# Kernel tuning notes

Measured on AMD Instinct MI355X. Metric: run time of the kernel, lower is better.

Reference implementation:

```python
import jax, jax.numpy as jnp
import numpy as np

NUM_HEADS = 16


def setup_inputs() -> dict:
    key = jax.random.key(0)
    ks = jax.random.split(key, 8)
    B, S, D = 2, 2048, 1024
    scale = 1.0 / np.sqrt(D)
    return {
        "v": jax.random.normal(ks[0], (B, S, D), jnp.float32),
        "k": jax.random.normal(ks[1], (B, S, D), jnp.float32),
        "q": jax.random.normal(ks[2], (B, S, D), jnp.float32),
        "mask": jnp.zeros((B, S), dtype=bool),  # True = masked (padding)
        "Wq": jax.random.normal(ks[3], (D, D), jnp.float32) * scale,
        "bq": jnp.zeros((D,), jnp.float32),
        "Wk": jax.random.normal(ks[4], (D, D), jnp.float32) * scale,
        "bk": jnp.zeros((D,), jnp.float32),
        "Wv": jax.random.normal(ks[5], (D, D), jnp.float32) * scale,
        "bv": jnp.zeros((D,), jnp.float32),
    }


def reference(v, k, q, mask, Wq, bq, Wk, bk, Wv, bv):
    B, Sq, D = q.shape
    H = NUM_HEADS
    hd = D // H

    def proj(x, W, b):
        # torch Linear: x @ W.T + b ; then split heads -> [B, H, S, hd]
        y = jnp.einsum("bsd,ed->bse", x, W) + b
        return y.reshape(B, -1, H, hd).transpose(0, 2, 1, 3)

    qh = proj(q, Wq, bq)  # [B,H,Sq,hd]
    kh = proj(k, Wk, bk)  # [B,H,Sk,hd]
    vh = proj(v, Wv, bv)  # [B,H,Sk,hd]

    scores = jnp.einsum("bhqd,bhkd->bhqk", qh, kh) / jnp.sqrt(
        jnp.asarray(hd, jnp.float32)
    )
    m = mask[:, None, None, :]  # add_dims -> [B,1,1,Sk]
    scores = jnp.where(m, -jnp.inf, scores)
    w = jax.nn.softmax(scores, axis=-1)
    w = jnp.where(m, 0.0, w)

    out = jnp.einsum("bhqk,bhkd->bhqd", w, vh)
    return out.transpose(0, 2, 1, 3).reshape(B, Sq, D)
```

## Files before the change

kernel.cpp:

```cpp
#include <hip/hip_runtime.h>
#include <hip/hip_bf16.h>
#include <cstdint>

typedef __attribute__((ext_vector_type(8))) short bf16x8;
typedef __attribute__((ext_vector_type(4))) float f32x4;

#define PLDT 72
#define KLDT 72

static __device__ __forceinline__ unsigned short f2bf(float x) {
    __hip_bfloat16 h = __float2bfloat16(x);
    union { __hip_bfloat16 b; unsigned short u; } c; c.b = h; return c.u;
}
static __device__ __forceinline__ float bf2f(unsigned short b) {
    union { float f; uint32_t u; } v; v.u = ((uint32_t)b) << 16;
    return v.f;
}
static __device__ __forceinline__ float exp2b(float x) {
    return __builtin_amdgcn_exp2f(x);
}
static __device__ __forceinline__ unsigned int cvt_pk_bf16(float lo, float hi) {
    unsigned int r;
    asm("v_cvt_pk_bf16_f32 %0, %1, %2" : "=v"(r) : "v"(lo), "v"(hi));
    return r;
}
static __device__ __forceinline__ void gload_lds16(const unsigned short* g, unsigned short* l) {
    __builtin_amdgcn_global_load_lds(
        (const __attribute__((address_space(1))) void*)g,
        (__attribute__((address_space(3))) void*)l, 16, 0, 0);
}

__global__ __launch_bounds__(256) void cvt_all(
    const float* __restrict__ xq, const float* __restrict__ xk, const float* __restrict__ xv,
    const float* __restrict__ wq, const float* __restrict__ wk, const float* __restrict__ wv,
    unsigned short* __restrict__ oxq, unsigned short* __restrict__ oxk, unsigned short* __restrict__ oxv,
    unsigned short* __restrict__ owq, unsigned short* __restrict__ owk, unsigned short* __restrict__ owv) {
    const int z = blockIdx.z;
    const float* in = (z == 0) ? xq : (z == 1) ? xk : (z == 2) ? xv
                      : (z == 3) ? wq : (z == 4) ? wk : wv;
    unsigned short* out = (z == 0) ? oxq : (z == 1) ? oxk : (z == 2) ? oxv
                          : (z == 3) ? owq : (z == 4) ? owk : owv;
    const int n8 = (z < 3) ? 524288 : 131072;
    int i = blockIdx.x * 256 + threadIdx.x;
    if (i >= n8) return;
    const float4* ip = (const float4*)in;
    float4 a = ip[2 * i];
    float4 b = ip[2 * i + 1];
    uint4 r;
    r.x = cvt_pk_bf16(a.x, a.y);
    r.y = cvt_pk_bf16(a.z, a.w);
    r.z = cvt_pk_bf16(b.x, b.y);
    r.w = cvt_pk_bf16(b.z, b.w);
    *(uint4*)(out + (size_t)i * 8) = r;
}

__global__ __launch_bounds__(256) void proj_gemm_bf16(
    const unsigned short* __restrict__ Xqb, const unsigned short* __restrict__ Xkb,
    const unsigned short* __restrict__ Xvb,
    const unsigned short* __restrict__ Wqb, const unsigned short* __restrict__ Wkb,
    const unsigned short* __restrict__ Wvb,
    const float* __restrict__ bqp, const float* __restrict__ bkp, const float* __restrict__ bvp,
    unsigned short* __restrict__ dq, unsigned short* __restrict__ dk, unsigned short* __restrict__ dv) {
    __shared__ unsigned short a_lds[128 * 64];
    __shared__ unsigned short b_lds[128 * 64];

    const int z = blockIdx.z;
    const unsigned short* X = (z == 0) ? Xqb : (z == 1) ? Xkb : Xvb;
    const unsigned short* W = (z == 0) ? Wqb : (z == 1) ? Wkb : Wvb;
    const float* bias = (z == 0) ? bqp : (z == 1) ? bkp : bvp;
    unsigned short* dst = (z == 0) ? dq : (z == 1) ? dk : dv;
    const bool vtrans = (z == 2);

    const int tid = threadIdx.x;
    const int lane = tid & 63;
    const int w = tid >> 6;
    const int lr = lane & 15;
    const int lg = lane >> 4;
    const int m0 = blockIdx.x * 128;
    const int e0 = blockIdx.y * 128;
    const int wrow = (w >> 1) * 64;
    const int wcol = (w & 1) * 64;

    f32x4 acc[4][4] = {};

#pragma unroll 1
    for (int t = 0; t < 16; ++t) {
        const int k0 = t * 64;
        __syncthreads();
#pragma unroll
        for (int i = 0; i < 4; ++i) {
            int c = i * 256 + w * 64 + lane;
            int row = c >> 3;
            int col = (c & 7) * 8;
            gload_lds16(X + (size_t)(m0 + row) * 1024 + k0 + col,
                        a_lds + (size_t)(i * 256 + w * 64) * 8);
            gload_lds16(W + (size_t)(e0 + row) * 1024 + k0 + col,
                        b_lds + (size_t)(i * 256 + w * 64) * 8);
        }
        __syncthreads();

#pragma unroll
        for (int ks = 0; ks < 2; ++ks) {
            const int kk = ks * 32 + lg * 8;
            bf16x8 af[4], bfr[4];
#pragma unroll
            for (int mt = 0; mt < 4; ++mt)
                af[mt] = *(const bf16x8*)(a_lds + (wrow + mt * 16 + lr) * 64 + kk);
#pragma unroll
            for (int nt = 0; nt < 4; ++nt)
                bfr[nt] = *(const bf16x8*)(b_lds + (wcol + nt * 16 + lr) * 64 + kk);
            __builtin_amdgcn_s_setprio(1);
#pragma unroll
            for (int mt = 0; mt < 4; ++mt)
#pragma unroll
                for (int nt = 0; nt < 4; ++nt)
                    acc[mt][nt] = __builtin_amdgcn_mfma_f32_16x16x32_bf16(
                        af[mt], bfr[nt], acc[mt][nt], 0, 0, 0);
            __builtin_amdgcn_s_setprio(0);
        }
    }

    for (int mt = 0; mt < 4; ++mt)
        for (int nt = 0; nt < 4; ++nt)
            for (int i = 0; i < 4; ++i) {
                int m = m0 + wrow + mt * 16 + lg * 4 + i;
                int e = e0 + wcol + nt * 16 + lr;
                float val = acc[mt][nt][i] + bias[e];
                int b = m >> 11, s = m & 2047;
                int h = e >> 6, d = e & 63;
                if (vtrans)
                    dst[(((size_t)b * 16 + h) * 64 + d) * 2048 + s] = f2bf(val);
                else
                    dst[(((size_t)b * 16 + h) * 2048 + s) * 64 + d] = f2bf(val);
            }
}

__global__ __launch_bounds__(256) void attn_kernel(
    const unsigned short* __restrict__ Qh,
    const unsigned short* __restrict__ Kh,
    const unsigned short* __restrict__ VTh,
    const unsigned char* __restrict__ mask,
    float* __restrict__ Out) {
    __shared__ unsigned short k_lds[64 * KLDT];
    __shared__ unsigned short v_lds[64 * KLDT];
    __shared__ unsigned short pbuf[4][32 * PLDT];

    const int tid = threadIdx.x;
    const int lane = tid & 63;
    const int w = tid >> 6;
    const int lr = lane & 15;
    const int lg = lane >> 4;

    const int bid = blockIdx.x;
    const int wk = (bid & 7) * 64 + (bid >> 3);
    const int x = wk & 15;
    const int bh = wk >> 4;
    const int h = bh & 15;
    const int b = bh >> 4;
    const int q0 = x * 128;

    const size_t headoff = (((size_t)b * 16) + h) * 2048 * 64;
    const unsigned short* Qp = Qh + headoff;
    const unsigned short* Kp = Kh + headoff;
    const unsigned short* VTp = VTh + headoff;
    const unsigned char* maskp = mask + b * 2048;
    unsigned short* pw = pbuf[w];

    const int srow0 = tid >> 3;
    const int srow1 = srow0 + 32;
    const int sch = (tid & 7) * 8;

    const float qscale = 0.125f * 1.44269504088896340736f;
    bf16x8 qf[2][2];
#pragma unroll
    for (int qh = 0; qh < 2; ++qh) {
        int row = q0 + w * 32 + qh * 16 + lr;
#pragma unroll
        for (int ks = 0; ks < 2; ++ks) {
            bf16x8 t = *(const bf16x8*)(Qp + (size_t)row * 64 + ks * 32 + lg * 8);
#pragma unroll
            for (int j = 0; j < 8; ++j)
                t[j] = (short)f2bf(bf2f((unsigned short)t[j]) * qscale);
            qf[qh][ks] = t;
        }
    }

    f32x4 o[2][4] = {};
    float mrow[2] = {-INFINITY, -INFINITY};
    float lsum[2] = {0.f, 0.f};

    uint4 kr0 = *(const uint4*)(Kp + srow0 * 64 + sch);
    uint4 kr1 = *(const uint4*)(Kp + srow1 * 64 + sch);
    uint4 vr0 = *(const uint4*)(VTp + srow0 * 2048 + sch);
    uint4 vr1 = *(const uint4*)(VTp + srow1 * 2048 + sch);

#pragma unroll 1
    for (int t = 0; t < 32; ++t) {
        const int kv0 = t * 64;
        __syncthreads();
        *(uint4*)(k_lds + srow0 * KLDT + sch) = kr0;
        *(uint4*)(k_lds + srow1 * KLDT + sch) = kr1;
        *(uint4*)(v_lds + srow0 * KLDT + sch) = vr0;
        *(uint4*)(v_lds + srow1 * KLDT + sch) = vr1;
        __syncthreads();

        if (t < 31) {
            const int nv0 = kv0 + 64;
            kr0 = *(const uint4*)(Kp + (nv0 + srow0) * 64 + sch);
            kr1 = *(const uint4*)(Kp + (nv0 + srow1) * 64 + sch);
            vr0 = *(const uint4*)(VTp + srow0 * 2048 + nv0 + sch);
            vr1 = *(const uint4*)(VTp + srow1 * 2048 + nv0 + sch);
        }

        bf16x8 kf[2][4];
#pragma unroll
        for (int ks = 0; ks < 2; ++ks)
#pragma unroll
            for (int mt = 0; mt < 4; ++mt)
                kf[ks][mt] = *(const bf16x8*)(k_lds + (mt * 16 + lr) * KLDT + ks * 32 + lg * 8);

        f32x4 s[2][4] = {};
        __builtin_amdgcn_s_setprio(1);
#pragma unroll
        for (int ks = 0; ks < 2; ++ks)
#pragma unroll
            for (int mt = 0; mt < 4; ++mt) {
                s[0][mt] = __builtin_amdgcn_mfma_f32_16x16x32_bf16(kf[ks][mt], qf[0][ks], s[0][mt], 0, 0, 0);
                s[1][mt] = __builtin_amdgcn_mfma_f32_16x16x32_bf16(kf[ks][mt], qf[1][ks], s[1][mt], 0, 0, 0);
            }
        __builtin_amdgcn_s_setprio(0);

        unsigned long long mbits = __ballot(maskp[kv0 + lane] != 0);
        if (mbits) {
#pragma unroll
            for (int qh = 0; qh < 2; ++qh)
#pragma unroll
                for (int mt = 0; mt < 4; ++mt)
#pragma unroll
                    for (int i = 0; i < 4; ++i)
                        if ((mbits >> (mt * 16 + lg * 4 + i)) & 1ull) s[qh][mt][i] = -1e30f;
        }

#pragma unroll
        for (int qh = 0; qh < 2; ++qh) {
            float mx = s[qh][0][0];
#pragma unroll
            for (int mt = 0; mt < 4; ++mt)
#pragma unroll
                for (int i = 0; i < 4; ++i) mx = fmaxf(mx, s[qh][mt][i]);
            mx = fmaxf(mx, __shfl_xor(mx, 16));
            mx = fmaxf(mx, __shfl_xor(mx, 32));
            if (!__all(mx <= mrow[qh] + 8.0f)) {
                float nm = fmaxf(mrow[qh], mx);
                float f = exp2b(mrow[qh] - nm);
                mrow[qh] = nm;
                lsum[qh] *= f;
#pragma unroll
                for (int mt = 0; mt < 4; ++mt)
#pragma unroll
                    for (int i = 0; i < 4; ++i) o[qh][mt][i] *= f;
            }
            float p[4][4];
            float ls = 0.f;
#pragma unroll
            for (int mt = 0; mt < 4; ++mt)
#pragma unroll
                for (int i = 0; i < 4; ++i) {
                    p[mt][i] = exp2b(s[qh][mt][i] - mrow[qh]);
                    ls += p[mt][i];
                }
            ls += __shfl_xor(ls, 16);
            ls += __shfl_xor(ls, 32);
            lsum[qh] += ls;

#pragma unroll
            for (int mt = 0; mt < 4; ++mt) {
                uint2 pr;
                pr.x = cvt_pk_bf16(p[mt][0], p[mt][1]);
                pr.y = cvt_pk_bf16(p[mt][2], p[mt][3]);
                *(uint2*)(&pw[(qh * 16 + lr) * PLDT + mt * 16 + lg * 4]) = pr;
            }
        }

        bf16x8 vf[2][4];
#pragma unroll
        for (int ks = 0; ks < 2; ++ks)
#pragma unroll
            for (int mt = 0; mt < 4; ++mt)
                vf[ks][mt] = *(const bf16x8*)(v_lds + (mt * 16 + lr) * KLDT + ks * 32 + lg * 8);

        __builtin_amdgcn_s_setprio(1);
#pragma unroll
        for (int qh = 0; qh < 2; ++qh)
#pragma unroll
            for (int ks = 0; ks < 2; ++ks) {
                bf16x8 pfr = *(const bf16x8*)(&pw[(qh * 16 + lr) * PLDT + ks * 32 + lg * 8]);
#pragma unroll
                for (int mt = 0; mt < 4; ++mt)
                    o[qh][mt] = __builtin_amdgcn_mfma_f32_16x16x32_bf16(vf[ks][mt], pfr, o[qh][mt], 0, 0, 0);
            }
        __builtin_amdgcn_s_setprio(0);
    }

    float* ep = (float*)pw;
#pragma unroll
    for (int qh = 0; qh < 2; ++qh) {
        float rinv = 1.0f / lsum[qh];
#pragma unroll
        for (int mt = 0; mt < 4; ++mt)
#pragma unroll
            for (int i = 0; i < 4; ++i)
                ep[lr * 68 + mt * 16 + lg * 4 + i] = o[qh][mt][i] * rinv;
#pragma unroll
        for (int j = 0; j < 4; ++j) {
            int id = lane + 64 * j;
            int row = id >> 4;
            int c4 = (id & 15) << 2;
            float4 val = *(const float4*)(&ep[row * 68 + c4]);
            *(float4*)(&Out[((size_t)b * 2048 + q0 + w * 32 + qh * 16 + row) * 1024 + h * 64 + c4]) = val;
        }
    }
}

extern "C" void kernel_launch(void* const* d_in, const int* in_sizes, int n_in,
                              void* d_out, int out_size, void* d_ws, size_t ws_size,
                              hipStream_t stream) {
    const float* v = (const float*)d_in[0];
    const float* k = (const float*)d_in[1];
    const float* q = (const float*)d_in[2];
    const unsigned char* mask = (const unsigned char*)d_in[3];
    const float* Wq = (const float*)d_in[4];
    const float* bq = (const float*)d_in[5];
    const float* Wk = (const float*)d_in[6];
    const float* bk = (const float*)d_in[7];
    const float* Wv = (const float*)d_in[8];
    const float* bv = (const float*)d_in[9];
    float* out = (float*)d_out;

    unsigned short* ws = (unsigned short*)d_ws;
    unsigned short* qh  = ws;
    unsigned short* kh  = ws + 4194304;
    unsigned short* vT  = ws + 8388608;
    unsigned short* xqb = ws + 12582912;
    unsigned short* xkb = ws + 16777216;
    unsigned short* xvb = ws + 20971520;
    unsigned short* wqb = ws + 25165824;
    unsigned short* wkb = ws + 26214400;
    unsigned short* wvb = ws + 27262976;

    cvt_all<<<dim3(2048, 1, 6), 256, 0, stream>>>(q, k, v, Wq, Wk, Wv,
                                                  xqb, xkb, xvb, wqb, wkb, wvb);

    dim3 pgrid(32, 8, 3);
    proj_gemm_bf16<<<pgrid, 256, 0, stream>>>(xqb, xkb, xvb, wqb, wkb, wvb,
                                              bq, bk, bv, qh, kh, vT);

    attn_kernel<<<dim3(512), 256, 0, stream>>>(qh, kh, vT, mask, out);
}
```

Measured before the change: 125.2 us.

## Use 8 waves of 16 query rows each with double-buffered K/V LDS

The attention kernel now runs 512 threads per block. Each of 8 waves handles 16 query rows instead of 32, and every thread stages one K row chunk and one V row chunk. K/V LDS tiles are double-buffered, which removes one of the two __syncthreads per KV tile. The aim is more waves in flight to hide latency and less barrier cost. In exchange, each wave reuses K/V fragments across fewer query rows, so there is more LDS read traffic per unit of MFMA work.

```diff
diff --git a/kernel.cpp b/kernel.cpp
--- a/kernel.cpp
+++ b/kernel.cpp
@@ -135,15 +135,14 @@
             }
 }
 
-__global__ __launch_bounds__(256) void attn_kernel(
+__global__ __launch_bounds__(512) void attn_kernel(
     const unsigned short* __restrict__ Qh,
     const unsigned short* __restrict__ Kh,
     const unsigned short* __restrict__ VTh,
     const unsigned char* __restrict__ mask,
     float* __restrict__ Out) {
-    __shared__ unsigned short k_lds[64 * KLDT];
-    __shared__ unsigned short v_lds[64 * KLDT];
-    __shared__ unsigned short pbuf[4][32 * PLDT];
+    __shared__ unsigned short kv_lds[2][2][64 * KLDT];
+    __shared__ unsigned short pbuf[8][2176];
 
     const int tid = threadIdx.x;
     const int lane = tid & 63;
@@ -157,7 +156,7 @@
     const int bh = wk >> 4;
     const int h = bh & 15;
     const int b = bh >> 4;
-    const int q0 = x * 128;
+    const int q0 = x * 128 + w * 16;
 
     const size_t headoff = (((size_t)b * 16) + h) * 2048 * 64;
     const unsigned short* Qp = Qh + headoff;
@@ -166,120 +165,104 @@
     const unsigned char* maskp = mask + b * 2048;
     unsigned short* pw = pbuf[w];
 
-    const int srow0 = tid >> 3;
-    const int srow1 = srow0 + 32;
+    const int srow = tid >> 3;
     const int sch = (tid & 7) * 8;
 
     const float qscale = 0.125f * 1.44269504088896340736f;
-    bf16x8 qf[2][2];
-#pragma unroll
-    for (int qh = 0; qh < 2; ++qh) {
-        int row = q0 + w * 32 + qh * 16 + lr;
-#pragma unroll
-        for (int ks = 0; ks < 2; ++ks) {
-            bf16x8 t = *(const bf16x8*)(Qp + (size_t)row * 64 + ks * 32 + lg * 8);
-#pragma unroll
-            for (int j = 0; j < 8; ++j)
-                t[j] = (short)f2bf(bf2f((unsigned short)t[j]) * qscale);
-            qf[qh][ks] = t;
-        }
+    bf16x8 qf[2];
+#pragma unroll
+    for (int ks = 0; ks < 2; ++ks) {
+        bf16x8 t = *(const bf16x8*)(Qp + (size_t)(q0 + lr) * 64 + ks * 32 + lg * 8);
+#pragma unroll
+        for (int j = 0; j < 8; ++j)
+            t[j] = (short)f2bf(bf2f((unsigned short)t[j]) * qscale);
+        qf[ks] = t;
     }
 
-    f32x4 o[2][4] = {};
-    float mrow[2] = {-INFINITY, -INFINITY};
-    float lsum[2] = {0.f, 0.f};
-
-    uint4 kr0 = *(const uint4*)(Kp + srow0 * 64 + sch);
-    uint4 kr1 = *(const uint4*)(Kp + srow1 * 64 + sch);
-    uint4 vr0 = *(const uint4*)(VTp + srow0 * 2048 + sch);
-    uint4 vr1 = *(const uint4*)(VTp + srow1 * 2048 + sch);
+    f32x4 o[4] = {};
+    float mrow = -INFINITY;
+    float lsum = 0.f;
+
+    uint4 kr = *(const uint4*)(Kp + srow * 64 + sch);
+    uint4 vr = *(const uint4*)(VTp + srow * 2048 + sch);
+    int cur = 0;
 
 #pragma unroll 1
     for (int t = 0; t < 32; ++t) {
         const int kv0 = t * 64;
-        __syncthreads();
-        *(uint4*)(k_lds + srow0 * KLDT + sch) = kr0;
-        *(uint4*)(k_lds + srow1 * KLDT + sch) = kr1;
-        *(uint4*)(v_lds + srow0 * KLDT + sch) = vr0;
-        *(uint4*)(v_lds + srow1 * KLDT + sch) = vr1;
+        *(uint4*)(&kv_lds[cur][0][srow * KLDT + sch]) = kr;
+        *(uint4*)(&kv_lds[cur][1][srow * KLDT + sch]) = vr;
         __syncthreads();
 
         if (t < 31) {
             const int nv0 = kv0 + 64;
-            kr0 = *(const uint4*)(Kp + (nv0 + srow0) * 64 + sch);
-            kr1 = *(const uint4*)(Kp + (nv0 + srow1) * 64 + sch);
-            vr0 = *(const uint4*)(VTp + srow0 * 2048 + nv0 + sch);
-            vr1 = *(const uint4*)(VTp + srow1 * 2048 + nv0 + sch);
-        }
+            kr = *(const uint4*)(Kp + (nv0 + srow) * 64 + sch);
+            vr = *(const uint4*)(VTp + srow * 2048 + nv0 + sch);
+        }
+
+        const unsigned short* kb = &kv_lds[cur][0][0];
+        const unsigned short* vb = &kv_lds[cur][1][0];
 
         bf16x8 kf[2][4];
 #pragma unroll
         for (int ks = 0; ks < 2; ++ks)
 #pragma unroll
             for (int mt = 0; mt < 4; ++mt)
-                kf[ks][mt] = *(const bf16x8*)(k_lds + (mt * 16 + lr) * KLDT + ks * 32 + lg * 8);
-
-        f32x4 s[2][4] = {};
+                kf[ks][mt] = *(const bf16x8*)(kb + (mt * 16 + lr) * KLDT + ks * 32 + lg * 8);
+
+        f32x4 s[4] = {};
         __builtin_amdgcn_s_setprio(1);
 #pragma unroll
         for (int ks = 0; ks < 2; ++ks)
 #pragma unroll
-            for (int mt = 0; mt < 4; ++mt) {
-                s[0][mt] = __builtin_amdgcn_mfma_f32_16x16x32_bf16(kf[ks][mt], qf[0][ks], s[0][mt], 0, 0, 0);
-                s[1][mt] = __builtin_amdgcn_mfma_f32_16x16x32_bf16(kf[ks][mt], qf[1][ks], s[1][mt], 0, 0, 0);
-            }
+            for (int mt = 0; mt < 4; ++mt)
+                s[mt] = __builtin_amdgcn_mfma_f32_16x16x32_bf16(kf[ks][mt], qf[ks], s[mt], 0, 0, 0);
         __builtin_amdgcn_s_setprio(0);
 
         unsigned long long mbits = __ballot(maskp[kv0 + lane] != 0);
         if (mbits) {
 #pragma unroll
-            for (int qh = 0; qh < 2; ++qh)
-#pragma unroll
-                for (int mt = 0; mt < 4; ++mt)
-#pragma unroll
-                    for (int i = 0; i < 4; ++i)
-                        if ((mbits >> (mt * 16 + lg * 4 + i)) & 1ull) s[qh][mt][i] = -1e30f;
-        }
-
-#pragma unroll
-        for (int qh = 0; qh < 2; ++qh) {
-            float mx = s[qh][0][0];
-#pragma unroll
-            for (int mt = 0; mt < 4; ++mt)
-#pragma unroll
-                for (int i = 0; i < 4; ++i) mx = fmaxf(mx, s[qh][mt][i]);
-            mx = fmaxf(mx, __shfl_xor(mx, 16));
-            mx = fmaxf(mx, __shfl_xor(mx, 32));
-            if (!__all(mx <= mrow[qh] + 8.0f)) {
-                float nm = fmaxf(mrow[qh], mx);
-                float f = exp2b(mrow[qh] - nm);
-                mrow[qh] = nm;
-                lsum[qh] *= f;
-#pragma unroll
-                for (int mt = 0; mt < 4; ++mt)
-#pragma unroll
-                    for (int i = 0; i < 4; ++i) o[qh][mt][i] *= f;
+            for (int mt = 0; mt < 4; ++mt)
+#pragma unroll
+                for (int i = 0; i < 4; ++i)
+                    if ((mbits >> (mt * 16 + lg * 4 + i)) & 1ull) s[mt][i] = -1e30f;
+        }
+
+        float mx = fmaxf(fmaxf(fmaxf(s[0][0], s[0][1]), fmaxf(s[0][2], s[0][3])),
+                         fmaxf(fmaxf(s[1][0], s[1][1]), fmaxf(s[1][2], s[1][3])));
+        mx = fmaxf(mx, fmaxf(fmaxf(fmaxf(s[2][0], s[2][1]), fmaxf(s[2][2], s[2][3])),
+                             fmaxf(fmaxf(s[3][0], s[3][1]), fmaxf(s[3][2], s[3][3]))));
+        mx = fmaxf(mx, __shfl_xor(mx, 16));
+        mx = fmaxf(mx, __shfl_xor(mx, 32));
+        if (!__all(mx <= mrow + 8.0f)) {
+            float nm = fmaxf(mrow, mx);
+            float f = exp2b(mrow - nm);
+            mrow = nm;
+            lsum *= f;
+#pragma unroll
+            for (int mt = 0; mt < 4; ++mt)
+#pragma unroll
+                for (int i = 0; i < 4; ++i) o[mt][i] *= f;
+        }
+        float p[4][4];
+        float ls = 0.f;
+#pragma unroll
+        for (int mt = 0; mt < 4; ++mt)
+#pragma unroll
+            for (int i = 0; i < 4; ++i) {
+                p[mt][i] = exp2b(s[mt][i] - mrow);
+                ls += p[mt][i];
             }
-            float p[4][4];
-            float ls = 0.f;
-#pragma unroll
-            for (int mt = 0; mt < 4; ++mt)
-#pragma unroll
-                for (int i = 0; i < 4; ++i) {
-                    p[mt][i] = exp2b(s[qh][mt][i] - mrow[qh]);
-                    ls += p[mt][i];
-                }
-            ls += __shfl_xor(ls, 16);
-            ls += __shfl_xor(ls, 32);
-            lsum[qh] += ls;
-
-#pragma unroll
-            for (int mt = 0; mt < 4; ++mt) {
-                uint2 pr;
-                pr.x = cvt_pk_bf16(p[mt][0], p[mt][1]);
-                pr.y = cvt_pk_bf16(p[mt][2], p[mt][3]);
-                *(uint2*)(&pw[(qh * 16 + lr) * PLDT + mt * 16 + lg * 4]) = pr;
-            }
+        ls += __shfl_xor(ls, 16);
+        ls += __shfl_xor(ls, 32);
+        lsum += ls;
+
+#pragma unroll
+        for (int mt = 0; mt < 4; ++mt) {
+            uint2 pr;
+            pr.x = cvt_pk_bf16(p[mt][0], p[mt][1]);
+            pr.y = cvt_pk_bf16(p[mt][2], p[mt][3]);
+            *(uint2*)(&pw[lr * PLDT + mt * 16 + lg * 4]) = pr;
         }
 
         bf16x8 vf[2][4];
@@ -287,38 +270,35 @@
         for (int ks = 0; ks < 2; ++ks)
 #pragma unroll
             for (int mt = 0; mt < 4; ++mt)
-                vf[ks][mt] = *(const bf16x8*)(v_lds + (mt * 16 + lr) * KLDT + ks * 32 + lg * 8);
+                vf[ks][mt] = *(const bf16x8*)(vb + (mt * 16 + lr) * KLDT + ks * 32 + lg * 8);
 
         __builtin_amdgcn_s_setprio(1);
 #pragma unroll
-        for (int qh = 0; qh < 2; ++qh)
-#pragma unroll
-            for (int ks = 0; ks < 2; ++ks) {
-                bf16x8 pfr = *(const bf16x8*)(&pw[(qh * 16 + lr) * PLDT + ks * 32 + lg * 8]);
-#pragma unroll
-                for (int mt = 0; mt < 4; ++mt)
-                    o[qh][mt] = __builtin_amdgcn_mfma_f32_16x16x32_bf16(vf[ks][mt], pfr, o[qh][mt], 0, 0, 0);
-            }
+        for (int ks = 0; ks < 2; ++ks) {
+            bf16x8 pfr = *(const bf16x8*)(&pw[lr * PLDT + ks * 32 + lg * 8]);
+#pragma unroll
+            for (int mt = 0; mt < 4; ++mt)
+                o[mt] = __builtin_amdgcn_mfma_f32_16x16x32_bf16(vf[ks][mt], pfr, o[mt], 0, 0, 0);
+        }
         __builtin_amdgcn_s_setprio(0);
+
+        cur ^= 1;
     }
 
     float* ep = (float*)pw;
-#pragma unroll
-    for (int qh = 0; qh < 2; ++qh) {
-        float rinv = 1.0f / lsum[qh];
-#pragma unroll
-        for (int mt = 0; mt < 4; ++mt)
-#pragma unroll
-            for (int i = 0; i < 4; ++i)
-                ep[lr * 68 + mt * 16 + lg * 4 + i] = o[qh][mt][i] * rinv;
-#pragma unroll
-        for (int j = 0; j < 4; ++j) {
-            int id = lane + 64 * j;
-            int row = id >> 4;
-            int c4 = (id & 15) << 2;
-            float4 val = *(const float4*)(&ep[row * 68 + c4]);
-            *(float4*)(&Out[((size_t)b * 2048 + q0 + w * 32 + qh * 16 + row) * 1024 + h * 64 + c4]) = val;
-        }
+    float rinv = 1.0f / lsum;
+#pragma unroll
+    for (int mt = 0; mt < 4; ++mt)
+#pragma unroll
+        for (int i = 0; i < 4; ++i)
+            ep[lr * 68 + mt * 16 + lg * 4 + i] = o[mt][i] * rinv;
+#pragma unroll
+    for (int j = 0; j < 4; ++j) {
+        int id = lane + 64 * j;
+        int row = id >> 4;
+        int c4 = (id & 15) << 2;
+        float4 val = *(const float4*)(&ep[row * 68 + c4]);
+        *(float4*)(&Out[((size_t)b * 2048 + q0 + row) * 1024 + h * 64 + c4]) = val;
     }
 }
 
@@ -355,5 +335,5 @@
     proj_gemm_bf16<<<pgrid, 256, 0, stream>>>(xqb, xkb, xvb, wqb, wkb, wvb,
                                               bq, bk, bv, qh, kh, vT);
 
-    attn_kernel<<<dim3(512), 256, 0, stream>>>(qh, kh, vT, mask, out);
-}
+    attn_kernel<<<dim3(512), 512, 0, stream>>>(qh, kh, vT, mask, out);
+}
```

Result: no change. 124.0 us (-1.0%).
